# Kernel optimization log

Hardware: AMD Instinct MI355X
Metric: run time of the kernel (lower is better)

Reference implementation:

```python
import jax, jax.numpy as jnp
import numpy as np
import math

N = 4900      # hardcoded in source (hQ[708:4900])
N1 = 708      # hardcoded group-1 size
IN, OUT, HEADS = 512, 256, 4
HD = OUT // HEADS


def _ln(x, g, b, eps):
    mu = jnp.mean(x, axis=-1, keepdims=True)
    var = jnp.var(x, axis=-1, keepdims=True)
    return (x - mu) / jnp.sqrt(var + eps) * g + b


def setup_inputs() -> dict:
    key = jax.random.key(0)
    ks = jax.random.split(key, 24)
    s = 0.05
    nrm = lambda k, shp: jax.random.normal(k, shp, jnp.float32) * s
    return {
        "feature": jax.random.normal(ks[0], (N, IN), jnp.float32),
        "adj_mat": jax.random.uniform(ks[1], (N, N), jnp.float32),
        "r": jax.random.normal(ks[2], (4, 256), jnp.float32),
        "Wq": nrm(ks[3], (IN, OUT)), "bq": jnp.zeros((OUT,), jnp.float32),
        "Wk": nrm(ks[4], (IN, OUT)), "bk": jnp.zeros((OUT,), jnp.float32),
        "Wv": nrm(ks[5], (IN, OUT)), "bv": jnp.zeros((OUT,), jnp.float32),
        "Ww": nrm(ks[6], (IN, OUT)), "bw": jnp.zeros((OUT,), jnp.float32),
        "Wr": nrm(ks[7], (256, OUT)), "br": jnp.zeros((OUT,), jnp.float32),
        "Wbeta": nrm(ks[8], (2 * OUT, OUT)), "bbeta": jnp.zeros((OUT,), jnp.float32),
        "ln1_g": jnp.ones((OUT,), jnp.float32), "ln1_b": jnp.zeros((OUT,), jnp.float32),
        "w1": nrm(ks[9], (OUT, OUT)), "b1": jnp.zeros((OUT,), jnp.float32),
        "ln2_g": jnp.ones((OUT,), jnp.float32), "ln2_b": jnp.zeros((OUT,), jnp.float32),
        "w2": nrm(ks[10], (OUT, OUT)),
        "flag": 1,
    }


def reference(feature, adj_mat, r, Wq, bq, Wk, bk, Wv, bv, Ww, bw, Wr, br,
              Wbeta, bbeta, ln1_g, ln1_b, w1, b1, ln2_g, ln2_b, w2, flag):
    H = feature @ Ww + bw                     # [N, OUT]
    rp = r @ Wr + br                          # [4, OUT]
    hQ = feature @ Wq + bq
    hK = feature @ Wk + bk
    hV = (feature @ Wv + bv).reshape(HEADS, N, HD)  # raw block reshape, as in source
    ridx = 1 if flag else 0
    # relation-modulated Q/K blocks; .view == raw reshape in the original
    hQ11 = (hQ[:N1] * rp[ridx]).reshape(HEADS, N1, HD)
    hK11 = (hK[:N1] * rp[ridx]).reshape(HEADS, N1, HD)
    hQ12 = (hQ[:N1] * rp[2]).reshape(HEADS, N1, HD)
    hQ21 = (hQ[N1:] * rp[2]).reshape(HEADS, N - N1, HD)
    hQ22 = (hQ[N1:] * rp[3]).reshape(HEADS, N - N1, HD)
    hK12 = (hK[:N1] * rp[2]).reshape(HEADS, N1, HD)
    hK21 = (hK[N1:] * rp[2]).reshape(HEADS, N - N1, HD)
    hK22 = (hK[N1:] * rp[3]).reshape(HEADS, N - N1, HD)
    a11 = jnp.einsum('hqd,hkd->hqk', hQ11, hK11)
    a12 = jnp.einsum('hqd,hkd->hqk', hQ12, hK21)
    a21 = jnp.einsum('hqd,hkd->hqk', hQ21, hK12)
    a22 = jnp.einsum('hqd,hkd->hqk', hQ22, hK22)
    alpha = jnp.concatenate([jnp.concatenate([a11, a12], axis=2),
                             jnp.concatenate([a21, a22], axis=2)], axis=1)
    alpha = alpha / math.sqrt(HEADS)          # source divides by sqrt(heads)
    alpha = alpha @ adj_mat                   # [HEADS, N, N] @ [N, N]
    # torch nn.Softmax() legacy default dim for 3D input is dim=0
    alpha = jax.nn.softmax(alpha, axis=0)
    m = alpha @ hV                            # [HEADS, N, HD]
    m = jnp.transpose(m, (1, 0, 2)).reshape(N, OUT)
    m = _ln(jax.nn.relu(m), ln1_g, ln1_b, 1e-5)
    beta = jax.nn.sigmoid(jnp.concatenate([H, m], axis=1) @ Wbeta + bbeta)
    out = beta * m + (1.0 - beta) * H
    h = jnp.tanh(_ln(out @ w1 + b1, ln2_g, ln2_b, 1e-6))
    return h @ w2
```

## Files before the change

kernel.cpp:

```cpp
#include <hip/hip_runtime.h>
#include <hip/hip_bf16.h>
#include <math.h>

#define NPOS 4900
#define NG1  708
#define NG2  4192
#define INF  512
#define OUTF 256
#define JBP  4928
#define NJT  154
#define NC   6
#define JTT  26
#define LDS_KS 36
#define PCH   2508800
#define KSPL 2112

typedef __attribute__((ext_vector_type(8))) short short8;
typedef __attribute__((ext_vector_type(16))) float f32x16;

__global__ __launch_bounds__(256) void k0_rp(
    const float* __restrict__ r, const float* __restrict__ Wr,
    const float* __restrict__ br, const int* __restrict__ flagp,
    float* __restrict__ S)
{
    __shared__ float rsh[1024];
    int t = threadIdx.x;
    for (int i = t; i < 1024; i += 256) rsh[i] = r[i];
    __syncthreads();
    float a0 = 0.f, a1 = 0.f, a2 = 0.f, a3 = 0.f;
    for (int c = 0; c < 256; ++c) {
        float w = Wr[c * 256 + t];
        a0 += rsh[c] * w;
        a1 += rsh[256 + c] * w;
        a2 += rsh[512 + c] * w;
        a3 += rsh[768 + c] * w;
    }
    float b = br[t];
    a0 += b; a1 += b; a2 += b; a3 += b;
    int ridx = (flagp[0] != 0) ? 1 : 0;
    S[t]         = ridx ? a1 : a0;
    S[256 + t]   = a2;
    S[512 + t]   = a3;
}

__global__ __launch_bounds__(256) void k1_proj(
    const float* __restrict__ feat,
    const float* __restrict__ Wq, const float* __restrict__ bq,
    const float* __restrict__ Wk, const float* __restrict__ bk,
    const float* __restrict__ Wv, const float* __restrict__ bv,
    const float* __restrict__ Ww, const float* __restrict__ bw,
    float* __restrict__ hQ, float* __restrict__ hK,
    float* __restrict__ hV, float* __restrict__ Hb)
{
    __shared__ float AT[16][68];
    __shared__ float Bs[16][132];
    int t = threadIdx.x;
    int mat = blockIdx.x >> 1;
    int n0  = (blockIdx.x & 1) * 128;
    int m0  = blockIdx.y * 64;
    const float* W; const float* bias; float* dst;
    switch (mat) {
        case 0:  W = Wq; bias = bq; dst = hQ; break;
        case 1:  W = Wk; bias = bk; dst = hK; break;
        case 2:  W = Wv; bias = bv; dst = hV; break;
        default: W = Ww; bias = bw; dst = Hb; break;
    }
    float acc[4][8];
#pragma unroll
    for (int i = 0; i < 4; ++i)
#pragma unroll
        for (int j = 0; j < 8; ++j) acc[i][j] = 0.f;
    int mg = (t >> 4) * 4, jg = (t & 15) * 8;
    int am = t & 63, ak = (t >> 6) * 4;
    int bkk = t >> 4, bn = (t & 15) * 8;
    for (int k0 = 0; k0 < INF; k0 += 16) {
        __syncthreads();
        {
            int row = m0 + am;
            float4 v = make_float4(0.f, 0.f, 0.f, 0.f);
            if (row < NPOS) v = *(const float4*)(feat + (size_t)row * INF + k0 + ak);
            AT[ak + 0][am] = v.x; AT[ak + 1][am] = v.y;
            AT[ak + 2][am] = v.z; AT[ak + 3][am] = v.w;
        }
        {
            const float* p = W + (size_t)(k0 + bkk) * OUTF + n0 + bn;
            float4 u0 = *(const float4*)p;
            float4 u1 = *(const float4*)(p + 4);
            *(float4*)&Bs[bkk][bn]     = u0;
            *(float4*)&Bs[bkk][bn + 4] = u1;
        }
        __syncthreads();
#pragma unroll
        for (int kk = 0; kk < 16; ++kk) {
            float4 a  = *(const float4*)&AT[kk][mg];
            float4 b0 = *(const float4*)&Bs[kk][jg];
            float4 b1 = *(const float4*)&Bs[kk][jg + 4];
            float av[4] = {a.x, a.y, a.z, a.w};
            float bv_[8] = {b0.x, b0.y, b0.z, b0.w, b1.x, b1.y, b1.z, b1.w};
#pragma unroll
            for (int i = 0; i < 4; ++i)
#pragma unroll
                for (int j = 0; j < 8; ++j) acc[i][j] += av[i] * bv_[j];
        }
    }
#pragma unroll
    for (int i = 0; i < 4; ++i) {
        int row = m0 + mg + i;
        if (row < NPOS) {
#pragma unroll
            for (int j = 0; j < 8; ++j) {
                int n = n0 + jg + j;
                dst[(size_t)row * OUTF + n] = acc[i][j] + bias[n];
            }
        }
    }
}

__device__ __forceinline__ void split2(float x0, float x1,
                                       unsigned& hi, unsigned& lo)
{
    unsigned u0 = __float_as_uint(x0), u1 = __float_as_uint(x1);
    unsigned h0 = u0 & 0xFFFF0000u,   h1 = u1 & 0xFFFF0000u;
    float r0 = x0 - __uint_as_float(h0);
    float r1 = x1 - __uint_as_float(h1);
    hi = (h0 >> 16) | h1;
    lo = (__float_as_uint(r0) >> 16) | (__float_as_uint(r1) & 0xFFFF0000u);
}

__device__ __forceinline__ void split1(float x, unsigned short& hi, unsigned short& lo)
{
    unsigned u = __float_as_uint(x);
    unsigned h = u & 0xFFFF0000u;
    float r = x - __uint_as_float(h);
    hi = (unsigned short)(h >> 16);
    lo = (unsigned short)(__float_as_uint(r) >> 16);
}

__device__ __forceinline__ short8 ldfrag(const unsigned short* base, int row, int kuo)
{
    const unsigned long long* p =
        (const unsigned long long*)(base + row * LDS_KS + kuo);
    union { unsigned long long q[2]; short8 s; } u;
    u.q[0] = p[0];
    u.q[1] = p[1];
    return u.s;
}

__device__ __forceinline__ short8 g16(const unsigned short* p)
{
    union { uint4 q; short8 s; } u;
    u.q = *(const uint4*)p;
    return u.s;
}

__device__ __forceinline__ short8 lds16u(const unsigned short* p)
{
    union { unsigned long long q[2]; short8 s; } u;
    u.q[0] = ((const unsigned long long*)p)[0];
    u.q[1] = ((const unsigned long long*)p)[1];
    return u.s;
}

__global__ __launch_bounds__(256) void k2_mfma(
    const float* __restrict__ hK, const float* __restrict__ adj,
    const float* __restrict__ S,
    float* __restrict__ P0, float* __restrict__ P1)
{
    __shared__ unsigned short sAh[128 * LDS_KS];
    __shared__ unsigned short sAl[128 * LDS_KS];
    __shared__ unsigned short sBh[64 * LDS_KS];
    __shared__ unsigned short sBl[64 * LDS_KS];

    int t = threadIdx.x;
    int j0 = blockIdx.x * 64;
    int h  = blockIdx.y;
    int chunk = blockIdx.z;
    int part = (chunk == 0) ? 0 : 1;
    int kbeg = (chunk <= 1) ? 0 : KSPL;
    int kend = (chunk == 0) ? NG1 : ((chunk == 2) ? NG2 : KSPL);
    int L = part ? NG2 : NG1;
    const float* kflat = hK + (part ? (size_t)NG1 * OUTF : 0);
    int rowoff = part ? NG1 : 0;
    float* Pout = chunk ? (P1 + (size_t)(chunk - 1) * PCH) : P0;

    int dd = t & 63;
    int kg = t >> 6;
    int jcol = j0 + dd;

    float sc[2][4];
#pragma unroll
    for (int g = 0; g < 2; ++g)
#pragma unroll
        for (int c = 0; c < 4; ++c)
            sc[g][c] = 0.5f * S[(g + part) * 256 + c * 64 + dd];

    f32x16 acc0, acc1;
#pragma unroll
    for (int i = 0; i < 16; ++i) { acc0[i] = 0.f; acc1[i] = 0.f; }

    int lane = t & 63;
    int half = lane >> 5;
    int ml = lane & 31;
    int arow = kg * 32 + ml;

    unsigned* uAh = (unsigned*)sAh;
    unsigned* uAl = (unsigned*)sAl;
    unsigned* uBh = (unsigned*)sBh;
    unsigned* uBl = (unsigned*)sBl;

    int ks0 = kbeg >> 5;
    int ks1 = (kend + 31) >> 5;
    for (int ks = ks0; ks < ks1; ++ks) {
        int k0 = ks * 32;
        float xa[8], xb[8];
#pragma unroll
        for (int i = 0; i < 8; ++i) {
            int kv = k0 + kg * 8 + i;
            bool okk = (kv < kend);
            xa[i] = okk ? kflat[(size_t)(h * L + kv) * 64 + dd] : 0.f;
            xb[i] = (okk && jcol < NPOS)
                        ? adj[(size_t)(rowoff + kv) * NPOS + jcol] : 0.f;
        }
        unsigned hA0[4], lA0[4], hA1[4], lA1[4], hB[4], lB[4];
#pragma unroll
        for (int i = 0; i < 8; i += 2) {
            float a0 = xa[i] * sc[0][i & 3];
            float a1 = xa[i + 1] * sc[0][(i + 1) & 3];
            split2(a0, a1, hA0[i >> 1], lA0[i >> 1]);
            float c0 = xa[i] * sc[1][i & 3];
            float c1 = xa[i + 1] * sc[1][(i + 1) & 3];
            split2(c0, c1, hA1[i >> 1], lA1[i >> 1]);
            split2(xb[i], xb[i + 1], hB[i >> 1], lB[i >> 1]);
        }
        __syncthreads();
        {
            int b0 = dd * 18 + kg * 4;
            int b1 = (64 + dd) * 18 + kg * 4;
            *(uint2*)(uAh + b0)     = make_uint2(hA0[0], hA0[1]);
            *(uint2*)(uAh + b0 + 2) = make_uint2(hA0[2], hA0[3]);
            *(uint2*)(uAl + b0)     = make_uint2(lA0[0], lA0[1]);
            *(uint2*)(uAl + b0 + 2) = make_uint2(lA0[2], lA0[3]);
            *(uint2*)(uAh + b1)     = make_uint2(hA1[0], hA1[1]);
            *(uint2*)(uAh + b1 + 2) = make_uint2(hA1[2], hA1[3]);
            *(uint2*)(uAl + b1)     = make_uint2(lA1[0], lA1[1]);
            *(uint2*)(uAl + b1 + 2) = make_uint2(lA1[2], lA1[3]);
            *(uint2*)(uBh + b0)     = make_uint2(hB[0], hB[1]);
            *(uint2*)(uBh + b0 + 2) = make_uint2(hB[2], hB[3]);
            *(uint2*)(uBl + b0)     = make_uint2(lB[0], lB[1]);
            *(uint2*)(uBl + b0 + 2) = make_uint2(lB[2], lB[3]);
        }
        __syncthreads();
#pragma unroll
        for (int kq = 0; kq < 2; ++kq) {
            int kuo = kq * 16 + half * 8;
            short8 aH = ldfrag(sAh, arow, kuo);
            short8 aL = ldfrag(sAl, arow, kuo);
            short8 b0H = ldfrag(sBh, ml, kuo);
            short8 b0L = ldfrag(sBl, ml, kuo);
            short8 b1H = ldfrag(sBh, 32 + ml, kuo);
            short8 b1L = ldfrag(sBl, 32 + ml, kuo);
            acc0 = __builtin_amdgcn_mfma_f32_32x32x16_bf16(aH, b0H, acc0, 0, 0, 0);
            acc0 = __builtin_amdgcn_mfma_f32_32x32x16_bf16(aH, b0L, acc0, 0, 0, 0);
            acc0 = __builtin_amdgcn_mfma_f32_32x32x16_bf16(aL, b0H, acc0, 0, 0, 0);
            acc1 = __builtin_amdgcn_mfma_f32_32x32x16_bf16(aH, b1H, acc1, 0, 0, 0);
            acc1 = __builtin_amdgcn_mfma_f32_32x32x16_bf16(aH, b1L, acc1, 0, 0, 0);
            acc1 = __builtin_amdgcn_mfma_f32_32x32x16_bf16(aL, b1H, acc1, 0, 0, 0);
        }
    }

    int col0 = j0 + ml;
    int col1 = j0 + 32 + ml;
#pragma unroll
    for (int reg = 0; reg < 16; ++reg) {
        int m = kg * 32 + (reg & 3) + 8 * (reg >> 2) + 4 * half;
        int g = m >> 6, ddm = m & 63;
        size_t rb = (size_t)((h * 2 + g) * 64 + ddm) * NPOS;
        Pout[rb + col0] = acc0[reg];
        if (col1 < NPOS) Pout[rb + col1] = acc1[reg];
    }
}

__global__ __launch_bounds__(256) void k2_reduce(
    const float* __restrict__ P0, const float* __restrict__ P1,
    unsigned short* __restrict__ Bhi, unsigned short* __restrict__ Blo)
{
    int t = threadIdx.x;
    int j = blockIdx.x * 256 + t;
    if (j >= JBP) return;
    int p = blockIdx.y;
    int g = p >> 2, h = p & 3;
    int kg = blockIdx.z;
    int k0 = kg * 16;
    int rowb = (h * 2 + g) * 64;

    unsigned short hi[16], lo[16];
    if (j < NPOS) {
        if (k0 < 64) {
#pragma unroll
            for (int i = 0; i < 16; ++i) {
                float v = P0[(size_t)(rowb + k0 + i) * NPOS + j];
                split1(v, hi[i], lo[i]);
            }
        } else {
#pragma unroll
            for (int i = 0; i < 16; ++i) {
                size_t off = (size_t)(rowb + (k0 - 64) + i) * NPOS + j;
                float v = P1[off] + P1[off + PCH];
                split1(v, hi[i], lo[i]);
            }
        }
    } else {
#pragma unroll
        for (int i = 0; i < 16; ++i) { hi[i] = 0; lo[i] = 0; }
    }
    int jt = j >> 5, mlr = j & 31;
    size_t fb = (((size_t)p * NJT + jt) * 8 + kg) * 512;
    union { unsigned short us[16]; uint4 v[2]; } uh, ul;
#pragma unroll
    for (int i = 0; i < 16; ++i) { uh.us[i] = hi[i]; ul.us[i] = lo[i]; }
    *(uint4*)(Bhi + fb + (size_t)mlr * 8)       = uh.v[0];
    *(uint4*)(Bhi + fb + 256 + (size_t)mlr * 8) = uh.v[1];
    *(uint4*)(Blo + fb + (size_t)mlr * 8)       = ul.v[0];
    *(uint4*)(Blo + fb + 256 + (size_t)mlr * 8) = ul.v[1];
}

__global__ __launch_bounds__(256) void qsplit(
    const float* __restrict__ hQ, const float* __restrict__ S,
    unsigned short* __restrict__ Qh, unsigned short* __restrict__ Ql)
{
    int t = threadIdx.x;
    int row = blockIdx.x * 2 + (t >> 7);
    int k = t & 127;
    int g, h, ql, Lg, vbase;
    if (row < 3072) { g = 0; h = row / 768; ql = row - h * 768; Lg = NG1; vbase = 0; }
    else {
        int rr = row - 3072;
        g = 1; h = rr / 4224; ql = rr - h * 4224; Lg = NG2; vbase = NG1 * OUTF;
    }
    int d = k & 63, p = k >> 6;
    float v = 0.f;
    if (ql < Lg)
        v = hQ[vbase + (size_t)(h * Lg + ql) * 64 + d] *
            S[(g + p) * 256 + (ql & 3) * 64 + d];
    unsigned short hi, lo;
    split1(v, hi, lo);
    Qh[(size_t)row * 128 + k] = hi;
    Ql[(size_t)row * 128 + k] = lo;
}

__global__ __launch_bounds__(256) void vtsplit(
    const float* __restrict__ hV,
    unsigned short* __restrict__ VtH, unsigned short* __restrict__ VtL)
{
    __shared__ float ls[128 * 65];
    int t = threadIdx.x;
    int j0 = blockIdx.x * 128;
    int h  = blockIdx.y;
#pragma unroll
    for (int i = 0; i < 32; ++i) {
        int idx = t + i * 256;
        int j = idx >> 6, d = idx & 63;
        float v = 0.f;
        int jg = j0 + j;
        if (jg < NPOS) v = hV[(size_t)(h * NPOS + jg) * 64 + d];
        ls[j * 65 + d] = v;
    }
    __syncthreads();
    int jtbase = j0 >> 5;
#pragma unroll
    for (int it = 0; it < 4; ++it) {
        int chunk = t + it * 256;
        int jtl = chunk >> 8;
        int r = chunk & 255;
        int ck = r >> 7;
        int r2 = r & 127;
        int nt = r2 >> 6;
        int l = r2 & 63;
        int jt = jtbase + jtl;
        if (jt < NJT) {
            int d = nt * 32 + (l & 31);
            int jloc = jtl * 32 + ck * 16 + (l >> 5) * 8;
            union { unsigned short us[8]; uint4 v; } uh, ul;
#pragma unroll
            for (int i = 0; i < 8; ++i)
                split1(ls[(jloc + i) * 65 + d], uh.us[i], ul.us[i]);
            size_t fb = ((((size_t)h * NJT + jt) * 2 + ck) * 2 + nt) * 512 + (size_t)l * 8;
            *(uint4*)(VtH + fb) = uh.v;
            *(uint4*)(VtL + fb) = ul.v;
        }
    }
}

__global__ __launch_bounds__(256, 2) void k3f_attn(
    const unsigned short* __restrict__ Qh, const unsigned short* __restrict__ Ql,
    const unsigned short* __restrict__ Bhi, const unsigned short* __restrict__ Blo,
    const unsigned short* __restrict__ VtH, const unsigned short* __restrict__ VtL,
    float* __restrict__ mpart)
{
    __shared__ __align__(16) char smem[35328];
    float* La = (float*)smem;
    unsigned short* Aa = (unsigned short*)(smem + 16896);

    int t = threadIdx.x;
    int w = t >> 6, lane = t & 63;
    int half = lane >> 5, ml = lane & 31;
    int h = w;

    int x = blockIdx.x;
    int c = blockIdx.y;
    int g = (x < 23) ? 0 : 1;
    int tile = g ? (x - 23) : x;
    int Lg = g ? NG2 : NG1;
    int posbase = g ? NG1 : 0;
    int qbase = g ? 3072 : 0;
    int hstr = g ? 4224 : 768;
    int q0 = tile * 32;

    const unsigned short* qrowH = Qh + (size_t)(qbase + h * hstr + q0 + ml) * 128 + half * 8;
    const unsigned short* qrowL = Ql + (size_t)(qbase + h * hstr + q0 + ml) * 128 + half * 8;
    short8 qfH[8], qfL[8];
#pragma unroll
    for (int kc = 0; kc < 8; ++kc) {
        qfH[kc] = g16(qrowH + kc * 16);
        qfL[kc] = g16(qrowL + kc * 16);
    }

    const unsigned short* bfH = Bhi + (size_t)(g * 4 + h) * NJT * 4096 + (size_t)lane * 8;
    const unsigned short* bfL = Blo + (size_t)(g * 4 + h) * NJT * 4096 + (size_t)lane * 8;
    const unsigned short* vfH = VtH + (size_t)h * NJT * 2048 + (size_t)lane * 8;
    const unsigned short* vfL = VtL + (size_t)h * NJT * 2048 + (size_t)lane * 8;

    f32x16 pv[2];
#pragma unroll
    for (int n = 0; n < 2; ++n)
#pragma unroll
        for (int r = 0; r < 16; ++r) pv[n][r] = 0.f;

    int spos = t >> 3, sj4 = (t & 7) * 4;

    int jt0 = c * JTT, jt1 = jt0 + JTT;
    if (jt1 > NJT) jt1 = NJT;

    short8 bbH[8];
#pragma unroll
    for (int kc = 0; kc < 8; ++kc)
        bbH[kc] = g16(bfH + (size_t)jt0 * 4096 + kc * 512);

    for (int jt = jt0; jt < jt1; ++jt) {
        size_t jo = (size_t)jt * 4096;
        int jn = (jt + 1 < jt1) ? jt + 1 : jt;
        size_t jno = (size_t)jn * 4096;

        short8 bbL[8];
#pragma unroll
        for (int kc = 0; kc < 8; ++kc) bbL[kc] = g16(bfL + jo + kc * 512);

        f32x16 qka, qkb;
#pragma unroll
        for (int r = 0; r < 16; ++r) { qka[r] = 0.f; qkb[r] = 0.f; }
#pragma unroll
        for (int kc = 0; kc < 8; kc += 2) {
            qka = __builtin_amdgcn_mfma_f32_32x32x16_bf16(bbH[kc], qfH[kc], qka, 0, 0, 0);
            qka = __builtin_amdgcn_mfma_f32_32x32x16_bf16(bbH[kc], qfL[kc], qka, 0, 0, 0);
            qkb = __builtin_amdgcn_mfma_f32_32x32x16_bf16(bbH[kc + 1], qfH[kc + 1], qkb, 0, 0, 0);
            qkb = __builtin_amdgcn_mfma_f32_32x32x16_bf16(bbH[kc + 1], qfL[kc + 1], qkb, 0, 0, 0);
        }
#pragma unroll
        for (int kc = 0; kc < 8; ++kc) bbH[kc] = g16(bfH + jno + kc * 512);

#pragma unroll
        for (int kc = 0; kc < 8; kc += 2) {
            qka = __builtin_amdgcn_mfma_f32_32x32x16_bf16(bbL[kc], qfH[kc], qka, 0, 0, 0);
            qkb = __builtin_amdgcn_mfma_f32_32x32x16_bf16(bbL[kc + 1], qfH[kc + 1], qkb, 0, 0, 0);
        }

        short8 vt[8];
        size_t vo = (size_t)jt * 2048;
#pragma unroll
        for (int q2 = 0; q2 < 4; ++q2) {
            vt[q2]     = g16(vfH + vo + q2 * 512);
            vt[4 + q2] = g16(vfL + vo + q2 * 512);
        }

#pragma unroll
        for (int r = 0; r < 16; ++r) {
            int jrow = (r & 3) + 8 * (r >> 2) + 4 * half;
            La[(w * 32 + jrow) * 33 + ml] = qka[r] + qkb[r];
        }
        __syncthreads();
        {
            unsigned short hi_[4][4], lo_[4][4];
#pragma unroll
            for (int jj = 0; jj < 4; ++jj) {
                int j = sj4 + jj;
                float v0 = La[(0 * 32 + j) * 33 + spos];
                float v1 = La[(1 * 32 + j) * 33 + spos];
                float v2 = La[(2 * 32 + j) * 33 + spos];
                float v3 = La[(3 * 32 + j) * 33 + spos];
                float mx = fmaxf(fmaxf(v0, v1), fmaxf(v2, v3));
                float e0 = __expf(v0 - mx), e1 = __expf(v1 - mx);
                float e2 = __expf(v2 - mx), e3 = __expf(v3 - mx);
                float inv = 1.0f / (e0 + e1 + e2 + e3);
                split1(e0 * inv, hi_[0][jj], lo_[0][jj]);
                split1(e1 * inv, hi_[1][jj], lo_[1][jj]);
                split1(e2 * inv, hi_[2][jj], lo_[2][jj]);
                split1(e3 * inv, hi_[3][jj], lo_[3][jj]);
            }
#pragma unroll
            for (int hh = 0; hh < 4; ++hh) {
                unsigned long long Hw =
                    (unsigned long long)hi_[hh][0] |
                    ((unsigned long long)hi_[hh][1] << 16) |
                    ((unsigned long long)hi_[hh][2] << 32) |
                    ((unsigned long long)hi_[hh][3] << 48);
                unsigned long long Lw =
                    (unsigned long long)lo_[hh][0] |
                    ((unsigned long long)lo_[hh][1] << 16) |
                    ((unsigned long long)lo_[hh][2] << 32) |
                    ((unsigned long long)lo_[hh][3] << 48);
                *(unsigned long long*)&Aa[((hh * 2 + 0) * 32 + spos) * 36 + sj4] = Hw;
                *(unsigned long long*)&Aa[((hh * 2 + 1) * 32 + spos) * 36 + sj4] = Lw;
            }
        }
        __syncthreads();
        const unsigned short* aBH = Aa + (size_t)((w * 2 + 0) * 32 + ml) * 36 + half * 8;
        const unsigned short* aBL = Aa + (size_t)((w * 2 + 1) * 32 + ml) * 36 + half * 8;
#pragma unroll
        for (int ck = 0; ck < 2; ++ck) {
            short8 paH = lds16u(aBH + ck * 16);
            short8 paL = lds16u(aBL + ck * 16);
            short8 w0H = vt[ck * 2 + 0];
            short8 w1H = vt[ck * 2 + 1];
            short8 w0L = vt[4 + ck * 2 + 0];
            short8 w1L = vt[4 + ck * 2 + 1];
            pv[0] = __builtin_amdgcn_mfma_f32_32x32x16_bf16(w0H, paH, pv[0], 0, 0, 0);
            pv[0] = __builtin_amdgcn_mfma_f32_32x32x16_bf16(w0H, paL, pv[0], 0, 0, 0);
            pv[0] = __builtin_amdgcn_mfma_f32_32x32x16_bf16(w0L, paH, pv[0], 0, 0, 0);
            pv[1] = __builtin_amdgcn_mfma_f32_32x32x16_bf16(w1H, paH, pv[1], 0, 0, 0);
            pv[1] = __builtin_amdgcn_mfma_f32_32x32x16_bf16(w1H, paL, pv[1], 0, 0, 0);
            pv[1] = __builtin_amdgcn_mfma_f32_32x32x16_bf16(w1L, paH, pv[1], 0, 0, 0);
        }
    }

    __syncthreads();
    float* scr = (float*)smem + w * 2112;
#pragma unroll
    for (int nt = 0; nt < 2; ++nt)
#pragma unroll
        for (int r = 0; r < 16; ++r) {
            int drow = (r & 3) + 8 * (r >> 2) + 4 * half;
            scr[ml * 66 + nt * 32 + drow] = pv[nt][r];
        }
    float* mpc = mpart + (size_t)c * NPOS * OUTF;
#pragma unroll 4
    for (int i = 0; i < 32; ++i) {
        int pg = q0 + i;
        if (pg < Lg)
            mpc[(size_t)(posbase + pg) * OUTF + h * 64 + lane] = scr[i * 66 + lane];
    }
}

__global__ __launch_bounds__(256) void e1_relu_ln(
    const float* __restrict__ mpart, const float* __restrict__ Hb,
    const float* __restrict__ g1, const float* __restrict__ b1,
    float* __restrict__ cc)
{
    int w = threadIdx.x >> 6, lane = threadIdx.x & 63;
    int row = blockIdx.x * 4 + w;
    int c = lane * 4;
    const size_t CST = (size_t)NPOS * OUTF;
    float4 x0 = *(const float4*)(mpart + (size_t)row * OUTF + c);
#pragma unroll
    for (int k = 1; k < NC; ++k) {
        float4 a = *(const float4*)(mpart + k * CST + (size_t)row * OUTF + c);
        x0.x += a.x; x0.y += a.y; x0.z += a.z; x0.w += a.w;
    }
    float x[4] = { fmaxf(x0.x, 0.f), fmaxf(x0.y, 0.f),
                   fmaxf(x0.z, 0.f), fmaxf(x0.w, 0.f) };
    float s = x[0] + x[1] + x[2] + x[3];
#pragma unroll
    for (int m = 32; m > 0; m >>= 1) s += __shfl_xor(s, m, 64);
    float mu = s * (1.0f / 256.0f);
    float vs = 0.f;
#pragma unroll
    for (int i = 0; i < 4; ++i) { float d = x[i] - mu; vs += d * d; }
#pragma unroll
    for (int m = 32; m > 0; m >>= 1) vs += __shfl_xor(vs, m, 64);
    float rs = rsqrtf(vs * (1.0f / 256.0f) + 1e-5f);
    float4 y;
    y.x = (x[0] - mu) * rs * g1[c + 0] + b1[c + 0];
    y.y = (x[1] - mu) * rs * g1[c + 1] + b1[c + 1];
    y.z = (x[2] - mu) * rs * g1[c + 2] + b1[c + 2];
    y.w = (x[3] - mu) * rs * g1[c + 3] + b1[c + 3];
    *(float4*)(cc + (size_t)row * INF + OUTF + c) = y;
    float4 hh = *(const float4*)(Hb + (size_t)row * OUTF + c);
    *(float4*)(cc + (size_t)row * INF + c) = hh;
}

__global__ __launch_bounds__(256) void e2_beta(
    const float* __restrict__ cc, const float* __restrict__ Wb,
    const float* __restrict__ bb, float* __restrict__ outb)
{
    __shared__ float AT[16][68];
    __shared__ float Bs[16][132];
    int t = threadIdx.x;
    int n0 = blockIdx.x * 128;
    int m0 = blockIdx.y * 64;
    float acc[4][8];
#pragma unroll
    for (int i = 0; i < 4; ++i)
#pragma unroll
        for (int j = 0; j < 8; ++j) acc[i][j] = 0.f;
    int mg = (t >> 4) * 4, jg = (t & 15) * 8;
    int am = t & 63, ak = (t >> 6) * 4;
    int bkk = t >> 4, bn = (t & 15) * 8;
    for (int k0 = 0; k0 < INF; k0 += 16) {
        __syncthreads();
        {
            int row = m0 + am;
            float4 v = make_float4(0.f, 0.f, 0.f, 0.f);
            if (row < NPOS) v = *(const float4*)(cc + (size_t)row * INF + k0 + ak);
            AT[ak + 0][am] = v.x; AT[ak + 1][am] = v.y;
            AT[ak + 2][am] = v.z; AT[ak + 3][am] = v.w;
        }
        {
            const float* p = Wb + (size_t)(k0 + bkk) * OUTF + n0 + bn;
            float4 u0 = *(const float4*)p;
            float4 u1 = *(const float4*)(p + 4);
            *(float4*)&Bs[bkk][bn]     = u0;
            *(float4*)&Bs[bkk][bn + 4] = u1;
        }
        __syncthreads();
#pragma unroll
        for (int kk = 0; kk < 16; ++kk) {
            float4 a  = *(const float4*)&AT[kk][mg];
            float4 b0 = *(const float4*)&Bs[kk][jg];
            float4 b1 = *(const float4*)&Bs[kk][jg + 4];
            float av[4] = {a.x, a.y, a.z, a.w};
            float bv_[8] = {b0.x, b0.y, b0.z, b0.w, b1.x, b1.y, b1.z, b1.w};
#pragma unroll
            for (int i = 0; i < 4; ++i)
#pragma unroll
                for (int j = 0; j < 8; ++j) acc[i][j] += av[i] * bv_[j];
        }
    }
#pragma unroll
    for (int i = 0; i < 4; ++i) {
        int row = m0 + mg + i;
        if (row < NPOS) {
#pragma unroll
            for (int j = 0; j < 8; ++j) {
                int n = n0 + jg + j;
                float x = acc[i][j] + bb[n];
                float sg = 1.0f / (1.0f + __expf(-x));
                float m1v = cc[(size_t)row * INF + OUTF + n];
                float Hv  = cc[(size_t)row * INF + n];
                outb[(size_t)row * OUTF + n] = sg * m1v + (1.0f - sg) * Hv;
            }
        }
    }
}

__global__ __launch_bounds__(256) void e3_w1_ln2(
    const float* __restrict__ outb, const float* __restrict__ w1,
    const float* __restrict__ b1v, const float* __restrict__ g2,
    const float* __restrict__ b2v, float* __restrict__ h2o)
{
    __shared__ float As[16][260];
    __shared__ float Bs[16][260];
    __shared__ float red[16][17];
    int t = threadIdx.x;
    int m0 = blockIdx.x * 16;
    {
        int rr = t >> 4, c4 = (t & 15) * 4;
        int row = m0 + rr;
#pragma unroll
        for (int i = 0; i < 4; ++i) {
            int c = c4 + i * 64;
            float4 x = make_float4(0.f, 0.f, 0.f, 0.f);
            if (row < NPOS) x = *(const float4*)(outb + (size_t)row * OUTF + c);
            *(float4*)&As[rr][c] = x;
        }
    }
    int q = t & 15, dg = (t >> 4) * 16;
    float acc[16];
#pragma unroll
    for (int i = 0; i < 16; ++i) acc[i] = 0.f;
    for (int k0 = 0; k0 < 256; k0 += 16) {
        __syncthreads();
        {
            int kk = t >> 4, n16 = (t & 15) * 16;
#pragma unroll
            for (int i = 0; i < 4; ++i) {
                float4 x = *(const float4*)(w1 + (size_t)(k0 + kk) * OUTF + n16 + i * 4);
                *(float4*)&Bs[kk][n16 + i * 4] = x;
            }
        }
        __syncthreads();
#pragma unroll
        for (int kk = 0; kk < 16; ++kk) {
            float a = As[q][k0 + kk];
#pragma unroll
            for (int i = 0; i < 16; i += 4) {
                float4 b = *(const float4*)&Bs[kk][dg + i];
                acc[i + 0] += a * b.x; acc[i + 1] += a * b.y;
                acc[i + 2] += a * b.z; acc[i + 3] += a * b.w;
            }
        }
    }
    float x[16];
#pragma unroll
    for (int i = 0; i < 16; ++i) x[i] = acc[i] + b1v[dg + i];
    float ps = 0.f;
#pragma unroll
    for (int i = 0; i < 16; ++i) ps += x[i];
    __syncthreads();
    red[t >> 4][q] = ps;
    __syncthreads();
    float s = 0.f;
#pragma unroll
    for (int i = 0; i < 16; ++i) s += red[i][q];
    float mu = s * (1.0f / 256.0f);
    float pvv = 0.f;
#pragma unroll
    for (int i = 0; i < 16; ++i) { float d = x[i] - mu; pvv += d * d; }
    __syncthreads();
    red[t >> 4][q] = pvv;
    __syncthreads();
    float v = 0.f;
#pragma unroll
    for (int i = 0; i < 16; ++i) v += red[i][q];
    float rs = rsqrtf(v * (1.0f / 256.0f) + 1e-6f);
    int row = m0 + q;
    if (row < NPOS) {
#pragma unroll
        for (int i = 0; i < 16; ++i) {
            int n = dg + i;
            h2o[(size_t)row * OUTF + n] = tanhf((x[i] - mu) * rs * g2[n] + b2v[n]);
        }
    }
}

__global__ __launch_bounds__(256) void e4_final(
    const float* __restrict__ h2in, const float* __restrict__ w2,
    float* __restrict__ outp)
{
    __shared__ float AT[16][68];
    __shared__ float Bs[16][132];
    int t = threadIdx.x;
    int n0 = blockIdx.x * 128;
    int m0 = blockIdx.y * 64;
    float acc[4][8];
#pragma unroll
    for (int i = 0; i < 4; ++i)
#pragma unroll
        for (int j = 0; j < 8; ++j) acc[i][j] = 0.f;
    int mg = (t >> 4) * 4, jg = (t & 15) * 8;
    int am = t & 63, ak = (t >> 6) * 4;
    int bkk = t >> 4, bn = (t & 15) * 8;
    for (int k0 = 0; k0 < 256; k0 += 16) {
        __syncthreads();
        {
            int row = m0 + am;
            float4 v = make_float4(0.f, 0.f, 0.f, 0.f);
            if (row < NPOS) v = *(const float4*)(h2in + (size_t)row * OUTF + k0 + ak);
            AT[ak + 0][am] = v.x; AT[ak + 1][am] = v.y;
            AT[ak + 2][am] = v.z; AT[ak + 3][am] = v.w;
        }
        {
            const float* p = w2 + (size_t)(k0 + bkk) * OUTF + n0 + bn;
            float4 u0 = *(const float4*)p;
            float4 u1 = *(const float4*)(p + 4);
            *(float4*)&Bs[bkk][bn]     = u0;
            *(float4*)&Bs[bkk][bn + 4] = u1;
        }
        __syncthreads();
#pragma unroll
        for (int kk = 0; kk < 16; ++kk) {
            float4 a  = *(const float4*)&AT[kk][mg];
            float4 b0 = *(const float4*)&Bs[kk][jg];
            float4 b1 = *(const float4*)&Bs[kk][jg + 4];
            float av[4] = {a.x, a.y, a.z, a.w};
            float bv_[8] = {b0.x, b0.y, b0.z, b0.w, b1.x, b1.y, b1.z, b1.w};
#pragma unroll
            for (int i = 0; i < 4; ++i)
#pragma unroll
                for (int j = 0; j < 8; ++j) acc[i][j] += av[i] * bv_[j];
        }
    }
#pragma unroll
    for (int i = 0; i < 4; ++i) {
        int row = m0 + mg + i;
        if (row < NPOS) {
#pragma unroll
            for (int j = 0; j < 8; ++j) {
                outp[(size_t)row * OUTF + n0 + jg + j] = acc[i][j];
            }
        }
    }
}

extern "C" void kernel_launch(void* const* d_in, const int* in_sizes, int n_in,
                              void* d_out, int out_size, void* d_ws, size_t ws_size,
                              hipStream_t stream)
{
    const float* feature = (const float*)d_in[0];
    const float* adj   = (const float*)d_in[1];
    const float* r     = (const float*)d_in[2];
    const float* Wq    = (const float*)d_in[3];
    const float* bq    = (const float*)d_in[4];
    const float* Wk    = (const float*)d_in[5];
    const float* bk    = (const float*)d_in[6];
    const float* Wv    = (const float*)d_in[7];
    const float* bv    = (const float*)d_in[8];
    const float* Ww    = (const float*)d_in[9];
    const float* bw    = (const float*)d_in[10];
    const float* Wr    = (const float*)d_in[11];
    const float* br    = (const float*)d_in[12];
    const float* Wbeta = (const float*)d_in[13];
    const float* bbeta = (const float*)d_in[14];
    const float* ln1g  = (const float*)d_in[15];
    const float* ln1b  = (const float*)d_in[16];
    const float* w1    = (const float*)d_in[17];
    const float* b1    = (const float*)d_in[18];
    const float* ln2g  = (const float*)d_in[19];
    const float* ln2b  = (const float*)d_in[20];
    const float* w2    = (const float*)d_in[21];
    const int*   flag  = (const int*)d_in[22];
    float* out = (float*)d_out;

    char* ws = (char*)d_ws;
    unsigned short* Qh    = (unsigned short*)(ws + 0);
    unsigned short* Qlo   = (unsigned short*)(ws + 5111808);
    unsigned short* VtH   = (unsigned short*)(ws + 10223616);
    unsigned short* VtL   = (unsigned short*)(ws + 12746752);
    float*          Hb    = (float*)(ws + 15269888);
    float*          P0    = (float*)(ws + 20287488);
    float*          P1    = (float*)(ws + 30322688);
    float*          mpart = (float*)(ws + 20287488);
    unsigned short* Bhi   = (unsigned short*)(ws + 50393088);
    unsigned short* Blo   = (unsigned short*)(ws + 60485632);
    float*          hK    = (float*)(ws + 50393088);
    float*          hQ    = (float*)(ws + 60485632);
    float*          hV    = (float*)(ws + 65503232);
    float*          cc    = (float*)(ws + 0);
    float*          outb  = (float*)(ws + 10223616);
    float*          hh2   = (float*)(ws + 20287488);
    float*          S     = (float*)(ws + 70578176);

    k0_rp<<<1, 256, 0, stream>>>(r, Wr, br, flag, S);
    k1_proj<<<dim3(8, 77), 256, 0, stream>>>(feature, Wq, bq, Wk, bk, Wv, bv, Ww, bw,
                                             hQ, hK, hV, Hb);
    qsplit<<<9984, 256, 0, stream>>>(hQ, S, Qh, Qlo);
    vtsplit<<<dim3(39, 4), 256, 0, stream>>>(hV, VtH, VtL);
    k2_mfma<<<dim3(77, 4, 3), 256, 0, stream>>>(hK, adj, S, P0, P1);
    k2_reduce<<<dim3(20, 8, 8), 256, 0, stream>>>(P0, P1, Bhi, Blo);
    k3f_attn<<<dim3(154, NC), 256, 0, stream>>>(Qh, Qlo, Bhi, Blo, VtH, VtL, mpart);
    e1_relu_ln<<<1225, 256, 0, stream>>>(mpart, Hb, ln1g, ln1b, cc);
    e2_beta<<<dim3(2, 77), 256, 0, stream>>>(cc, Wbeta, bbeta, outb);
    e3_w1_ln2<<<307, 256, 0, stream>>>(outb, w1, b1, ln2g, ln2b, hh2);
    e4_final<<<dim3(2, 77), 256, 0, stream>>>(hh2, w2, out);
}
```

Baseline: 699.6 us.

## Precompute hK A-operand fragments in MFMA layout and raise attention occupancy

Adds an asplit kernel that scales hK by the relation vector, splits it into bf16 hi/lo, and stores it pre-swizzled in MFMA fragment order. k2_mfma then loads A fragments straight from global memory instead of recomputing the scale and split in every column block and staging through LDS. This removes redundant work repeated across 77 column blocks and frees LDS, at the cost of an extra launch and global traffic. Separately, k3f_attn launch bounds go from 2 to 3 blocks per SM, which may force register spilling.

```diff
diff --git a/kernel.cpp b/kernel.cpp
--- a/kernel.cpp
+++ b/kernel.cpp
@@ -14,6 +14,7 @@
 #define LDS_KS 36
 #define PCH   2508800
 #define KSPL 2112
+#define NFRAG 308
 
 typedef __attribute__((ext_vector_type(8))) short short8;
 typedef __attribute__((ext_vector_type(16))) float f32x16;
@@ -161,13 +162,41 @@
     return u.s;
 }
 
+__global__ __launch_bounds__(256) void asplit(
+    const float* __restrict__ hK, const float* __restrict__ S,
+    unsigned short* __restrict__ AFh, unsigned short* __restrict__ AFl)
+{
+    int t = threadIdx.x;
+    int p = blockIdx.y;
+    int h = p >> 2, mt = p & 3;
+    int f = blockIdx.x * 4 + (t >> 6);
+    int l = t & 63, ml = l & 31, half = l >> 5;
+    int part = (f < 46) ? 0 : 1;
+    int kbase = part ? (f - 46) * 16 : f * 16;
+    int L = part ? NG2 : NG1;
+    const float* kflat = hK + (part ? (size_t)NG1 * OUTF : 0);
+    int m = mt * 32 + ml;
+    int g = m >> 6, dd = m & 63;
+    const float* Sg = S + (g + part) * 256;
+    union { unsigned short us[8]; uint4 v; } uh, ul;
+#pragma unroll
+    for (int i = 0; i < 8; ++i) {
+        int kv = kbase + half * 8 + i;
+        float v = 0.f;
+        if (kv < L)
+            v = kflat[(size_t)(h * L + kv) * 64 + dd] * 0.5f * Sg[(kv & 3) * 64 + dd];
+        split1(v, uh.us[i], ul.us[i]);
+    }
+    size_t off = ((size_t)p * NFRAG + f) * 512 + (size_t)l * 8;
+    *(uint4*)(AFh + off) = uh.v;
+    *(uint4*)(AFl + off) = ul.v;
+}
+
 __global__ __launch_bounds__(256) void k2_mfma(
-    const float* __restrict__ hK, const float* __restrict__ adj,
-    const float* __restrict__ S,
+    const unsigned short* __restrict__ AFh, const unsigned short* __restrict__ AFl,
+    const float* __restrict__ adj,
     float* __restrict__ P0, float* __restrict__ P1)
 {
-    __shared__ unsigned short sAh[128 * LDS_KS];
-    __shared__ unsigned short sAl[128 * LDS_KS];
     __shared__ unsigned short sBh[64 * LDS_KS];
     __shared__ unsigned short sBl[64 * LDS_KS];
 
@@ -178,8 +207,6 @@
     int part = (chunk == 0) ? 0 : 1;
     int kbeg = (chunk <= 1) ? 0 : KSPL;
     int kend = (chunk == 0) ? NG1 : ((chunk == 2) ? NG2 : KSPL);
-    int L = part ? NG2 : NG1;
-    const float* kflat = hK + (part ? (size_t)NG1 * OUTF : 0);
     int rowoff = part ? NG1 : 0;
     float* Pout = chunk ? (P1 + (size_t)(chunk - 1) * PCH) : P0;
 
@@ -187,13 +214,6 @@
     int kg = t >> 6;
     int jcol = j0 + dd;
 
-    float sc[2][4];
-#pragma unroll
-    for (int g = 0; g < 2; ++g)
-#pragma unroll
-        for (int c = 0; c < 4; ++c)
-            sc[g][c] = 0.5f * S[(g + part) * 256 + c * 64 + dd];
-
     f32x16 acc0, acc1;
 #pragma unroll
     for (int i = 0; i < 16; ++i) { acc0[i] = 0.f; acc1[i] = 0.f; }
@@ -201,49 +221,32 @@
     int lane = t & 63;
     int half = lane >> 5;
     int ml = lane & 31;
-    int arow = kg * 32 + ml;
-
-    unsigned* uAh = (unsigned*)sAh;
-    unsigned* uAl = (unsigned*)sAl;
+
     unsigned* uBh = (unsigned*)sBh;
     unsigned* uBl = (unsigned*)sBl;
+
+    const unsigned short* afh = AFh + ((size_t)(h * 4 + kg) * NFRAG) * 512 + (size_t)lane * 8;
+    const unsigned short* afl = AFl + ((size_t)(h * 4 + kg) * NFRAG) * 512 + (size_t)lane * 8;
+    int fragoff = part ? 46 : 0;
 
     int ks0 = kbeg >> 5;
     int ks1 = (kend + 31) >> 5;
     for (int ks = ks0; ks < ks1; ++ks) {
         int k0 = ks * 32;
-        float xa[8], xb[8];
+        float xb[8];
 #pragma unroll
         for (int i = 0; i < 8; ++i) {
             int kv = k0 + kg * 8 + i;
-            bool okk = (kv < kend);
-            xa[i] = okk ? kflat[(size_t)(h * L + kv) * 64 + dd] : 0.f;
-            xb[i] = (okk && jcol < NPOS)
+            xb[i] = (kv < kend && jcol < NPOS)
                         ? adj[(size_t)(rowoff + kv) * NPOS + jcol] : 0.f;
         }
-        unsigned hA0[4], lA0[4], hA1[4], lA1[4], hB[4], lB[4];
-#pragma unroll
-        for (int i = 0; i < 8; i += 2) {
-            float a0 = xa[i] * sc[0][i & 3];
-            float a1 = xa[i + 1] * sc[0][(i + 1) & 3];
-            split2(a0, a1, hA0[i >> 1], lA0[i >> 1]);
-            float c0 = xa[i] * sc[1][i & 3];
-            float c1 = xa[i + 1] * sc[1][(i + 1) & 3];
-            split2(c0, c1, hA1[i >> 1], lA1[i >> 1]);
+        unsigned hB[4], lB[4];
+#pragma unroll
+        for (int i = 0; i < 8; i += 2)
             split2(xb[i], xb[i + 1], hB[i >> 1], lB[i >> 1]);
-        }
         __syncthreads();
         {
             int b0 = dd * 18 + kg * 4;
-            int b1 = (64 + dd) * 18 + kg * 4;
-            *(uint2*)(uAh + b0)     = make_uint2(hA0[0], hA0[1]);
-            *(uint2*)(uAh + b0 + 2) = make_uint2(hA0[2], hA0[3]);
-            *(uint2*)(uAl + b0)     = make_uint2(lA0[0], lA0[1]);
-            *(uint2*)(uAl + b0 + 2) = make_uint2(lA0[2], lA0[3]);
-            *(uint2*)(uAh + b1)     = make_uint2(hA1[0], hA1[1]);
-            *(uint2*)(uAh + b1 + 2) = make_uint2(hA1[2], hA1[3]);
-            *(uint2*)(uAl + b1)     = make_uint2(lA1[0], lA1[1]);
-            *(uint2*)(uAl + b1 + 2) = make_uint2(lA1[2], lA1[3]);
             *(uint2*)(uBh + b0)     = make_uint2(hB[0], hB[1]);
             *(uint2*)(uBh + b0 + 2) = make_uint2(hB[2], hB[3]);
             *(uint2*)(uBl + b0)     = make_uint2(lB[0], lB[1]);
@@ -252,9 +255,10 @@
         __syncthreads();
 #pragma unroll
         for (int kq = 0; kq < 2; ++kq) {
+            size_t fo = (size_t)(fragoff + 2 * ks + kq) * 512;
+            short8 aH = g16(afh + fo);
+            short8 aL = g16(afl + fo);
             int kuo = kq * 16 + half * 8;
-            short8 aH = ldfrag(sAh, arow, kuo);
-            short8 aL = ldfrag(sAl, arow, kuo);
             short8 b0H = ldfrag(sBh, ml, kuo);
             short8 b0L = ldfrag(sBl, ml, kuo);
             short8 b1H = ldfrag(sBh, 32 + ml, kuo);
@@ -391,7 +395,7 @@
     }
 }
 
-__global__ __launch_bounds__(256, 2) void k3f_attn(
+__global__ __launch_bounds__(256, 3) void k3f_attn(
     const unsigned short* __restrict__ Qh, const unsigned short* __restrict__ Ql,
     const unsigned short* __restrict__ Bhi, const unsigned short* __restrict__ Blo,
     const unsigned short* __restrict__ VtH, const unsigned short* __restrict__ VtL,
@@ -843,6 +847,8 @@
     float*          hK    = (float*)(ws + 50393088);
     float*          hQ    = (float*)(ws + 60485632);
     float*          hV    = (float*)(ws + 65503232);
+    unsigned short* AFh   = (unsigned short*)(ws + 60485632);
+    unsigned short* AFl   = (unsigned short*)(ws + 65531904);
     float*          cc    = (float*)(ws + 0);
     float*          outb  = (float*)(ws + 10223616);
     float*          hh2   = (float*)(ws + 20287488);
@@ -853,7 +859,8 @@
                                              hQ, hK, hV, Hb);
     qsplit<<<9984, 256, 0, stream>>>(hQ, S, Qh, Qlo);
     vtsplit<<<dim3(39, 4), 256, 0, stream>>>(hV, VtH, VtL);
-    k2_mfma<<<dim3(77, 4, 3), 256, 0, stream>>>(hK, adj, S, P0, P1);
+    asplit<<<dim3(77, 16), 256, 0, stream>>>(hK, S, AFh, AFl);
+    k2_mfma<<<dim3(77, 4, 3), 256, 0, stream>>>(AFh, AFl, adj, P0, P1);
     k2_reduce<<<dim3(20, 8, 8), 256, 0, stream>>>(P0, P1, Bhi, Blo);
     k3f_attn<<<dim3(154, NC), 256, 0, stream>>>(Qh, Qlo, Bhi, Blo, VtH, VtL, mpart);
     e1_relu_ln<<<1225, 256, 0, stream>>>(mpart, Hb, ln1g, ln1b, cc);
```

Result: slower. 873.6 us (+24.9%).
